# Kernel tuning notes

Measured on AMD Instinct MI355X. Metric: run time of the kernel, lower is better.

## Reference

```python
import jax, jax.numpy as jnp
import numpy as np

L = 12        # num_layers == seq_len
HORIZON = 6


def setup_inputs() -> dict:
    key = jax.random.key(0)
    k0, k1, k2, k3, k4 = jax.random.split(key, 5)
    B, N, T = 64, 1024, 12
    x = jax.random.normal(k0, (B, 1, N, T), jnp.float32)
    # hidden_size=1 -> PyTorch init is U(-1,1); use scaled normals
    w_ih = jax.random.normal(k1, (L, 3), jnp.float32) * 0.5
    w_hh = jax.random.normal(k2, (L, 3), jnp.float32) * 0.5
    b_ih = jax.random.normal(k3, (L, 3), jnp.float32) * 0.5
    b_hh = jax.random.normal(k4, (L, 3), jnp.float32) * 0.5
    return {"x": x, "w_ih": w_ih, "w_hh": w_hh, "b_ih": b_ih, "b_hh": b_hh}


def _gru_pass(seq, h0, w_ih, w_hh, b_ih, b_hh):
    # seq: [T, B, N] scalar inputs per step; h0: [L, B, N]
    def step(h, x_t):
        inp = x_t                       # [B, N]
        new_h = []
        for l in range(L):
            gi = inp[..., None] * w_ih[l] + b_ih[l]      # [B, N, 3]
            gh = h[l][..., None] * w_hh[l] + b_hh[l]     # [B, N, 3]
            r = jax.nn.sigmoid(gi[..., 0] + gh[..., 0])
            z = jax.nn.sigmoid(gi[..., 1] + gh[..., 1])
            n = jnp.tanh(gi[..., 2] + r * gh[..., 2])
            hn = (1.0 - z) * n + z * h[l]
            new_h.append(hn)
            inp = hn                    # output of layer l feeds layer l+1
        return jnp.stack(new_h), inp    # carry [L,B,N], top-layer output [B,N]
    h_final, outs = jax.lax.scan(step, h0, seq)
    return outs, h_final                # outs: [T, B, N]


def reference(x, w_ih, w_hh, b_ih, b_hh):
    # x: [B, 1, N, T]  (permute(0,2,3,1) in torch -> [B, N, T, 1])
    B, _, N, T = x.shape
    seq = jnp.transpose(x[:, 0], (2, 0, 1))   # [T, B, N]
    h = jnp.zeros((L, B, N), x.dtype)          # hidden=None -> zeros
    outs, h = _gru_pass(seq, h, w_ih, w_hh, b_ih, b_hh)
    for _ in range(HORIZON):
        outs, h = _gru_pass(outs, h, w_ih, w_hh, b_ih, b_hh)
    # torch builds result[i] = final hidden of layer i, shaped [B,1,N,1];
    # we return the stacked list: [L, B, 1, N, 1]
    return h[:, :, None, :, None]
```

## Files before the change

### kernel.cpp

```cpp
#include <hip/hip_runtime.h>

#define LNUM 12
#define TNUM 12
#define NPASS 7

__global__ __launch_bounds__(256, 1)
void gru_chain_kernel(const float* __restrict__ x,
                      const float* __restrict__ w_ih,
                      const float* __restrict__ w_hh,
                      const float* __restrict__ b_ih,
                      const float* __restrict__ b_hh,
                      float* __restrict__ out,
                      int total) {
    const int tid = blockIdx.x * blockDim.x + threadIdx.x;
    if (tid >= total) return;

    const float NL2E = -1.4426950408889634f;
    const float TL2E =  2.8853900817779268f;

    float wi0[LNUM], wi1[LNUM], wi2[LNUM];
    float wh0[LNUM], wh1[LNUM], wh2[LNUM];
    float b0[LNUM], b1[LNUM], bi2[LNUM], bh2[LNUM];
#pragma unroll
    for (int l = 0; l < LNUM; ++l) {
        wi0[l] = NL2E * w_ih[l*3+0];
        wi1[l] = NL2E * w_ih[l*3+1];
        wi2[l] = TL2E * w_ih[l*3+2];
        wh0[l] = NL2E * w_hh[l*3+0];
        wh1[l] = NL2E * w_hh[l*3+1];
        wh2[l] = TL2E * w_hh[l*3+2];
        b0[l]  = NL2E * (b_ih[l*3+0] + b_hh[l*3+0]);
        b1[l]  = NL2E * (b_ih[l*3+1] + b_hh[l*3+1]);
        bi2[l] = TL2E * b_ih[l*3+2];
        bh2[l] = TL2E * b_hh[l*3+2];
    }

    float seq[TNUM];
    const float4* xv = reinterpret_cast<const float4*>(x + (size_t)tid * TNUM);
#pragma unroll
    for (int i = 0; i < TNUM / 4; ++i) {
        float4 v = xv[i];
        seq[i*4+0] = v.x; seq[i*4+1] = v.y; seq[i*4+2] = v.z; seq[i*4+3] = v.w;
    }

    float h[LNUM];
#pragma unroll
    for (int l = 0; l < LNUM; ++l) h[l] = 0.0f;

#pragma unroll 1
    for (int p = 0; p < NPASS; ++p) {
#pragma unroll
        for (int t = 0; t < TNUM; ++t) {
            float inp = seq[t];
#pragma unroll
            for (int l = 0; l < LNUM; ++l) {
                float ar  = fmaf(inp, wi0[l], fmaf(h[l], wh0[l], b0[l]));
                float az  = fmaf(inp, wi1[l], fmaf(h[l], wh1[l], b1[l]));
                float gi2 = fmaf(inp,  wi2[l], bi2[l]);
                float gh2 = fmaf(h[l], wh2[l], bh2[l]);

                float er = __builtin_amdgcn_exp2f(ar);
                float ez = __builtin_amdgcn_exp2f(az);
                float r  = __builtin_amdgcn_rcpf(1.0f + er);
                float z  = __builtin_amdgcn_rcpf(1.0f + ez);

                float an = fmaf(r, gh2, gi2);
                float en = __builtin_amdgcn_exp2f(an);
                float u  = __builtin_amdgcn_rcpf(1.0f + en);
                float n  = fmaf(-2.0f, u, 1.0f);

                float hn = fmaf(z, h[l] - n, n);
                h[l] = hn;
                inp  = hn;
            }
            seq[t] = inp;
        }
    }

#pragma unroll
    for (int l = 0; l < LNUM; ++l) {
        out[(size_t)l * total + tid] = h[l];
    }
}

extern "C" void kernel_launch(void* const* d_in, const int* in_sizes, int n_in,
                              void* d_out, int out_size, void* d_ws, size_t ws_size,
                              hipStream_t stream) {
    const float* x    = (const float*)d_in[0];
    const float* w_ih = (const float*)d_in[1];
    const float* w_hh = (const float*)d_in[2];
    const float* b_ih = (const float*)d_in[3];
    const float* b_hh = (const float*)d_in[4];
    float* out = (float*)d_out;

    const int total = in_sizes[0] / TNUM;
    const int block = 256;
    const int grid  = (total + block - 1) / block;
    gru_chain_kernel<<<grid, block, 0, stream>>>(x, w_ih, w_hh, b_ih, b_hh, out, total);
}
```

Baseline: 107.1 us.

## Precompute scaled weights in prep kernel, share one reciprocal across sigmoid gates

```diff
diff --git a/kernel.cpp b/kernel.cpp
--- a/kernel.cpp
+++ b/kernel.cpp
@@ -4,35 +4,54 @@
 #define TNUM 12
 #define NPASS 7
 
+__global__ void gru_prep_kernel(const float* __restrict__ w_ih,
+                                const float* __restrict__ w_hh,
+                                const float* __restrict__ b_ih,
+                                const float* __restrict__ b_hh,
+                                float* __restrict__ ws) {
+    const float NL2E = -1.4426950408889634f;
+    const float TL2E =  2.8853900817779268f;
+    int j = threadIdx.x;
+    if (j >= 10 * LNUM) return;
+    int g = j / LNUM, l = j % LNUM;
+    float v;
+    switch (g) {
+        case 0: v = NL2E * w_ih[3*l+0]; break;
+        case 1: v = NL2E * w_ih[3*l+1]; break;
+        case 2: v = TL2E * w_ih[3*l+2]; break;
+        case 3: v = NL2E * w_hh[3*l+0]; break;
+        case 4: v = NL2E * w_hh[3*l+1]; break;
+        case 5: v = TL2E * w_hh[3*l+2]; break;
+        case 6: v = NL2E * (b_ih[3*l+0] + b_hh[3*l+0]); break;
+        case 7: v = NL2E * (b_ih[3*l+1] + b_hh[3*l+1]); break;
+        case 8: v = TL2E * b_ih[3*l+2]; break;
+        default: v = TL2E * b_hh[3*l+2]; break;
+    }
+    ws[j] = v;
+}
+
 __global__ __launch_bounds__(256, 1)
 void gru_chain_kernel(const float* __restrict__ x,
-                      const float* __restrict__ w_ih,
-                      const float* __restrict__ w_hh,
-                      const float* __restrict__ b_ih,
-                      const float* __restrict__ b_hh,
+                      const float* __restrict__ ws,
                       float* __restrict__ out,
                       int total) {
     const int tid = blockIdx.x * blockDim.x + threadIdx.x;
     if (tid >= total) return;
 
-    const float NL2E = -1.4426950408889634f;
-    const float TL2E =  2.8853900817779268f;
+    const float* __restrict__ wi0 = ws +   0;
+    const float* __restrict__ wi1 = ws +  12;
+    const float* __restrict__ wi2 = ws +  24;
+    const float* __restrict__ wh0 = ws +  36;
+    const float* __restrict__ wh1 = ws +  48;
+    const float* __restrict__ wh2 = ws +  60;
 
-    float wi0[LNUM], wi1[LNUM], wi2[LNUM];
-    float wh0[LNUM], wh1[LNUM], wh2[LNUM];
-    float b0[LNUM], b1[LNUM], bi2[LNUM], bh2[LNUM];
+    float vb0[LNUM], vb1[LNUM], vbi2[LNUM], vbh2[LNUM];
 #pragma unroll
     for (int l = 0; l < LNUM; ++l) {
-        wi0[l] = NL2E * w_ih[l*3+0];
-        wi1[l] = NL2E * w_ih[l*3+1];
-        wi2[l] = TL2E * w_ih[l*3+2];
-        wh0[l] = NL2E * w_hh[l*3+0];
-        wh1[l] = NL2E * w_hh[l*3+1];
-        wh2[l] = TL2E * w_hh[l*3+2];
-        b0[l]  = NL2E * (b_ih[l*3+0] + b_hh[l*3+0]);
-        b1[l]  = NL2E * (b_ih[l*3+1] + b_hh[l*3+1]);
-        bi2[l] = TL2E * b_ih[l*3+2];
-        bh2[l] = TL2E * b_hh[l*3+2];
+        vb0[l]  = ws[72  + l];
+        vb1[l]  = ws[84  + l];
+        vbi2[l] = ws[96  + l];
+        vbh2[l] = ws[108 + l];
     }
 
     float seq[TNUM];
@@ -54,22 +73,24 @@
             float inp = seq[t];
 #pragma unroll
             for (int l = 0; l < LNUM; ++l) {
-                float ar  = fmaf(inp, wi0[l], fmaf(h[l], wh0[l], b0[l]));
-                float az  = fmaf(inp, wi1[l], fmaf(h[l], wh1[l], b1[l]));
-                float gi2 = fmaf(inp,  wi2[l], bi2[l]);
-                float gh2 = fmaf(h[l], wh2[l], bh2[l]);
+                float ar = fmaf(inp, wi0[l], fmaf(h[l], wh0[l], vb0[l]));
+                float az = fmaf(inp, wi1[l], fmaf(h[l], wh1[l], vb1[l]));
+                float gn = fmaf(inp, wi2[l], vbi2[l]);
+                float hg = fmaf(h[l], wh2[l], vbh2[l]);
 
                 float er = __builtin_amdgcn_exp2f(ar);
                 float ez = __builtin_amdgcn_exp2f(az);
-                float r  = __builtin_amdgcn_rcpf(1.0f + er);
-                float z  = __builtin_amdgcn_rcpf(1.0f + ez);
+                float ea = 1.0f + er;
+                float eb = 1.0f + ez;
+                float D  = __builtin_amdgcn_rcpf(ea * eb);
+                float r  = D * eb;
+                float z  = D * ea;
 
-                float an = fmaf(r, gh2, gi2);
-                float en = __builtin_amdgcn_exp2f(an);
+                float en = __builtin_amdgcn_exp2f(fmaf(r, hg, gn));
                 float u  = __builtin_amdgcn_rcpf(1.0f + en);
                 float n  = fmaf(-2.0f, u, 1.0f);
 
-                float hn = fmaf(z, h[l] - n, n);
+                float hn = fmaf(z, h[l], fmaf(-z, n, n));
                 h[l] = hn;
                 inp  = hn;
             }
@@ -92,9 +113,12 @@
     const float* b_ih = (const float*)d_in[3];
     const float* b_hh = (const float*)d_in[4];
     float* out = (float*)d_out;
+    float* ws  = (float*)d_ws;
+
+    gru_prep_kernel<<<1, 128, 0, stream>>>(w_ih, w_hh, b_ih, b_hh, ws);
 
     const int total = in_sizes[0] / TNUM;
     const int block = 256;
     const int grid  = (total + block - 1) / block;
-    gru_chain_kernel<<<grid, block, 0, stream>>>(x, w_ih, w_hh, b_ih, b_hh, out, total);
+    gru_chain_kernel<<<grid, block, 0, stream>>>(x, ws, out, total);
 }
```

New measurement: 111.0 us. 3.6% more time.
